# Performance work log

Measured on AMD Instinct MI355X. Metric: run time of the kernel, lower is better.

The kernel has to match this reference:

```python
import jax, jax.numpy as jnp
import numpy as np

MUL = 128
LS = (0, 1, 2, 3, 4)
LMAX = 4
DIM = MUL * sum(2 * l + 1 for l in LS)   # 3200
NUM_IRREPS = MUL * len(LS)               # 640
NUM_M = [MUL * (LMAX + 1 - m) for m in range(LMAX + 1)]
N = 16384


def _expm(A, order=24, squarings=10):
    A = A / (2.0 ** squarings)
    E = np.eye(A.shape[0])
    T = np.eye(A.shape[0])
    for k in range(1, order):
        T = T @ A / k
        E = E + T
    for _ in range(squarings):
        E = E @ E
    return E


def _su2_generators(j):
    m = np.arange(-j, j)
    raising = np.diag(-np.sqrt(j * (j + 1) - m * (m + 1)), k=-1).astype(complex)
    m = np.arange(-j + 1, j + 1)
    lowering = np.diag(np.sqrt(j * (j + 1) - m * (m - 1)), k=1).astype(complex)
    m = np.arange(-j, j + 1)
    return np.stack([0.5 * (raising + lowering), np.diag(1j * m), -0.5j * (raising - lowering)])


def _q_real_to_complex(l):
    q = np.zeros((2 * l + 1, 2 * l + 1), dtype=complex)
    for m in range(-l, 0):
        q[l + m, l + abs(m)] = 1 / np.sqrt(2)
        q[l + m, l - abs(m)] = -1j / np.sqrt(2)
    q[l, l] = 1.0
    for m in range(1, l + 1):
        q[l + m, l + abs(m)] = (-1) ** m / np.sqrt(2)
        q[l + m, l - abs(m)] = 1j * (-1) ** m / np.sqrt(2)
    return (-1j) ** l * q


def _so3_generators(l):
    X = _su2_generators(l)
    Q = _q_real_to_complex(l)
    return np.real(np.conj(Q.T)[None] @ X @ Q[None])


def _J(l):
    # J_l = pi rotation about (x+y)/sqrt(2): conjugates z_rot (y-axis) into the beta (x-axis) rotation,
    # reproducing e3nn's _Jd used in wigner_D = Z(a) J Z(b) J Z(g).
    X = _so3_generators(l)
    return _expm(np.pi * (X[0] + X[1]) / np.sqrt(2.0))


JMAT = {l: jnp.asarray(_J(l), dtype=jnp.float32) for l in LS if l > 0}


def _build_mask():
    mask = np.zeros((LMAX + 1, DIM), dtype=bool)
    cur = 0
    for l in LS:
        for k in range(MUL):
            base = cur + k * (2 * l + 1)
            for m in range(l + 1):
                if m == 0:
                    mask[0, base + l] = True
                else:
                    mask[m, base + l + m] = True
                    mask[m, base + l - m] = True
        cur += MUL * (2 * l + 1)
    return mask


_MASK = _build_mask()
IDX = [np.nonzero(_MASK[m])[0] for m in range(LMAX + 1)]  # same layout for in and out irreps


def _z_rot(angle, l):
    d = 2 * l + 1
    freqs = jnp.arange(l, -l - 1, -1, dtype=angle.dtype)
    c = jnp.cos(freqs * angle[:, None])
    s = jnp.sin(freqs * angle[:, None])
    i = jnp.arange(d)
    M = jnp.zeros((angle.shape[0], d, d), angle.dtype)
    M = M.at[:, i, i].set(c)
    M = M.at[:, i, d - 1 - i].add(s)
    return M


def _wigner(l, alpha, beta, gamma):
    J = JMAT[l].astype(alpha.dtype)
    return _z_rot(alpha, l) @ J @ _z_rot(beta, l) @ J @ _z_rot(gamma, l)


def _forward(x, R, fc0_w, fc0_b, w_ms):
    n = x.shape[0]
    # xyz_to_angles(R[:, [1, 2, 0]])
    v = jnp.stack([R[:, 1], R[:, 2], R[:, 0]], axis=-1)
    v = v / jnp.clip(jnp.linalg.norm(v, axis=-1, keepdims=True), 1e-12)
    v = jnp.clip(v, -1.0, 1.0)
    beta = jnp.arccos(v[:, 1])
    alpha = jnp.arctan2(v[:, 0], v[:, 2])
    gamma = jnp.zeros_like(alpha)
    rots = {l: _wigner(l, alpha, beta, gamma) for l in LS if l > 0}
    # rotate input blocks; the l=0 block of x_rot stays zero (exactly as the torch source)
    parts = []
    off = 0
    for l in LS:
        d = 2 * l + 1
        size = MUL * d
        if l == 0:
            parts.append(jnp.zeros((n, size), x.dtype))
        else:
            blk = x[:, off:off + size].reshape(n, MUL, d)
            parts.append(jnp.einsum('nji,nmj->nmi', rots[l], blk).reshape(n, size))
        off += size
    x_rot = jnp.concatenate(parts, axis=1)
    out = jnp.zeros((n, DIM), x.dtype)
    # m = 0 path (radial_emb=False => w = ones, a no-op multiply)
    out = out.at[:, IDX[0]].add(x_rot[:, IDX[0]] @ fc0_w.T + fc0_b)
    # m >= 1 SO(2) paths
    for m in range(1, LMAX + 1):
        co = NUM_M[m]
        seg = x_rot[:, IDX[m]].reshape(n, 2, co)
        y = jnp.einsum('nct,ot->nco', seg, w_ms[m - 1])  # (n, 2, 2*co)
        re = y[:, 0, :co] - y[:, 1, co:]
        im = y[:, 0, co:] + y[:, 1, :co]
        out = out.at[:, IDX[m]].add(jnp.stack((re, im), axis=1).reshape(n, -1))
    # rotate output blocks (l=0 untouched)
    parts = []
    off = 0
    for l in LS:
        d = 2 * l + 1
        size = MUL * d
        blk = out[:, off:off + size]
        if l > 0:
            blk = jnp.einsum('nji,nmj->nmi', rots[l], blk.reshape(n, MUL, d)).reshape(n, size)
        parts.append(blk)
        off += size
    return jnp.concatenate(parts, axis=1)


def setup_inputs() -> dict:
    key = jax.random.key(0)
    ks = jax.random.split(key, 8)
    x = jax.random.normal(ks[0], (N, DIM), jnp.float32)
    R = jax.random.normal(ks[1], (N, 3), jnp.float32)
    fc0_w = jax.random.normal(ks[2], (NUM_IRREPS, NUM_IRREPS), jnp.float32) / np.float32(np.sqrt(NUM_IRREPS))
    fc0_b = jnp.zeros((NUM_IRREPS,), jnp.float32)
    w1 = jax.random.normal(ks[3], (2 * NUM_M[1], NUM_M[1]), jnp.float32) / np.float32(np.sqrt(2.0 * NUM_M[1]))
    w2 = jax.random.normal(ks[4], (2 * NUM_M[2], NUM_M[2]), jnp.float32) / np.float32(np.sqrt(2.0 * NUM_M[2]))
    w3 = jax.random.normal(ks[5], (2 * NUM_M[3], NUM_M[3]), jnp.float32) / np.float32(np.sqrt(2.0 * NUM_M[3]))
    w4 = jax.random.normal(ks[6], (2 * NUM_M[4], NUM_M[4]), jnp.float32) / np.float32(np.sqrt(2.0 * NUM_M[4]))
    return {"x": x, "R": R, "fc0_w": fc0_w, "fc0_b": fc0_b, "w1": w1, "w2": w2, "w3": w3, "w4": w4}


def reference(x, R, fc0_w, fc0_b, w1, w2, w3, w4):
    return _forward(x, R, fc0_w, fc0_b, (w1, w2, w3, w4))
```

## Files before the change

### kernel.cpp

```cpp
#include <hip/hip_runtime.h>
#include <hip/hip_bf16.h>
#include <math.h>

#define N_ROWS 16384
#define DIM    3200

using short8  = __attribute__((ext_vector_type(8))) short;
using floatx4 = __attribute__((ext_vector_type(4))) float;

__device__ const int c_K [5] = {640, 1024, 768, 512, 256};
__device__ const int c_UO[5] = {0, 640, 1664, 2432, 2944};
__device__ const int c_WO[5] = {0, 409600, 1458176, 2048000, 2310144};
__device__ const int c_mOf[25]  = {0,0,0,0,0, 1,1,1,1,1,1,1,1, 2,2,2,2,2,2, 3,3,3,3, 4,4};
__device__ const int c_ntOf[25] = {0,1,2,3,4, 0,1,2,3,4,5,6,7, 0,1,2,3,4,5, 0,1,2,3, 0,1};

__device__ __forceinline__ constexpr int joff_of(int l) { return l==1 ? 0 : l==2 ? 9 : l==3 ? 34 : 83; }
__device__ __forceinline__ constexpr int gO(int m)      { return m==1 ? 640 : m==2 ? 1664 : m==3 ? 2432 : 2944; }

__global__ __launch_bounds__(128) void build_J(float* __restrict__ Jout)
{
    const int l = blockIdx.x + 1;
    const int d = 2*l + 1;
    const int dd = d*d;
    const int tid = threadIdx.x;
    __shared__ double Qr[81], Qi[81], Xr[81], Xi[81];
    __shared__ double M1r[81], M1i[81];
    __shared__ double Am[81], Em[81], Tm[81], Tn[81];

    if (tid == 0) {
        for (int e = 0; e < dd; ++e) { Qr[e]=0; Qi[e]=0; Xr[e]=0; Xi[e]=0; }
        const double jj = (double)l;
        for (int i = 0; i < d-1; ++i) {
            double mm = -jj + (double)i;
            Xr[(i+1)*d + i] += 0.5 * (-sqrt(jj*(jj+1.0) - mm*(mm+1.0)));
            double m2 = -jj + 1.0 + (double)i;
            Xr[i*d + (i+1)] += 0.5 * ( sqrt(jj*(jj+1.0) - m2*(m2-1.0)));
        }
        for (int i = 0; i < d; ++i) Xi[i*d + i] = -jj + (double)i;
        const double is2 = 1.0 / sqrt(2.0);
        for (int mm = -l; mm < 0; ++mm) {
            int r = l + mm;
            Qr[r*d + (l - mm)] = is2;
            Qi[r*d + (l + mm)] = -is2;
        }
        Qr[l*d + l] = 1.0;
        for (int mm = 1; mm <= l; ++mm) {
            int r = l + mm;
            double sgn = (mm & 1) ? -1.0 : 1.0;
            Qr[r*d + (l + mm)] = sgn * is2;
            Qi[r*d + (l - mm)] = sgn * is2;
        }
        double fr, fi;
        switch (l & 3) {
            case 0: fr = 1;  fi = 0;  break;
            case 1: fr = 0;  fi = -1; break;
            case 2: fr = -1; fi = 0;  break;
            default: fr = 0; fi = 1;  break;
        }
        for (int e = 0; e < dd; ++e) {
            double qr = Qr[e], qi = Qi[e];
            Qr[e] = qr*fr - qi*fi;
            Qi[e] = qr*fi + qi*fr;
        }
    }
    __syncthreads();
    const int i = (d > 0) ? tid / d : 0;
    const int j = (d > 0) ? tid % d : 0;
    if (tid < dd) {
        double ar = 0, ai = 0;
        for (int k = 0; k < d; ++k) {
            double xr = Xr[i*d+k], xi = Xi[i*d+k];
            double qr = Qr[k*d+j], qi = Qi[k*d+j];
            ar += xr*qr - xi*qi;
            ai += xr*qi + xi*qr;
        }
        M1r[tid] = ar; M1i[tid] = ai;
    }
    __syncthreads();
    if (tid < dd) {
        double ar = 0;
        for (int k = 0; k < d; ++k)
            ar += Qr[k*d+i]*M1r[k*d+j] + Qi[k*d+i]*M1i[k*d+j];
        const double scale = 3.14159265358979323846 / sqrt(2.0) / 1024.0;
        Am[tid] = ar * scale;
        Em[tid] = (i == j) ? 1.0 : 0.0;
        Tm[tid] = (i == j) ? 1.0 : 0.0;
    }
    __syncthreads();
    for (int k = 1; k < 24; ++k) {
        if (tid < dd) {
            double s = 0;
            for (int b = 0; b < d; ++b) s += Tm[i*d+b] * Am[b*d+j];
            Tn[tid] = s / (double)k;
        }
        __syncthreads();
        if (tid < dd) { Tm[tid] = Tn[tid]; Em[tid] += Tn[tid]; }
        __syncthreads();
    }
    for (int s = 0; s < 10; ++s) {
        if (tid < dd) {
            double v = 0;
            for (int b = 0; b < d; ++b) v += Em[i*d+b] * Em[b*d+j];
            Tn[tid] = v;
        }
        __syncthreads();
        if (tid < dd) Em[tid] = Tn[tid];
        __syncthreads();
    }
    if (tid < dd) Jout[joff_of(l) + tid] = (float)Em[tid];
}

__global__ __launch_bounds__(256) void prep_w(
    const float* __restrict__ fc0_w,
    const float* __restrict__ w1, const float* __restrict__ w2,
    const float* __restrict__ w3, const float* __restrict__ w4,
    __hip_bfloat16* __restrict__ Wall)
{
    const int m = blockIdx.y;
    const int idx = blockIdx.x * 256 + threadIdx.x;
    if (m == 0) {
        if (idx < 640*640) Wall[idx] = __float2bfloat16(fc0_w[idx]);
        return;
    }
    const int co = 128 * (5 - m);
    const int C  = 2 * co;
    if (idx >= C*C) return;
    const float* wm = (m==1) ? w1 : (m==2) ? w2 : (m==3) ? w3 : w4;
    const int jj = idx / C;
    const int tt = idx - jj * C;
    float v;
    if (jj < co) {
        v = (tt < co) ? wm[jj*co + tt] : -wm[(co + jj)*co + (tt - co)];
    } else {
        v = (tt < co) ? wm[jj*co + tt] :  wm[(jj - co)*co + (tt - co)];
    }
    Wall[c_WO[m] + idx] = __float2bfloat16(v);
}

template<int L>
__device__ __forceinline__ void rot_channel(const float* xs, const float* Dm,
                                            __hip_bfloat16* Urow, int k)
{
    constexpr int d = 2*L + 1;
    const float* Dl = Dm + joff_of(L);
    const int xoff = 128*L*L + k*d;
    float y[d];
#pragma unroll
    for (int q = 0; q < d; ++q) {
        float acc = 0.f;
#pragma unroll
        for (int j = 0; j < d; ++j) acc += Dl[j*d + q] * xs[xoff + j];
        y[q] = acc;
    }
#pragma unroll
    for (int q = 0; q < d; ++q) {
        const int mp = q - L;
        int g;
        if (mp == 0) g = L*128 + k;
        else {
            const int mm = mp < 0 ? -mp : mp;
            g = gO(mm) + 2*((L - mm)*128 + k) + (mp > 0 ? 1 : 0);
        }
        Urow[g] = __float2bfloat16(y[q]);
    }
}

template<int L>
__device__ __forceinline__ void unrot_channel(const __hip_bfloat16* ys, const float* Dm,
                                              float* orow, int k)
{
    constexpr int d = 2*L + 1;
    float yv[d];
#pragma unroll
    for (int q = 0; q < d; ++q) {
        const int mp = q - L;
        int g;
        if (mp == 0) g = L*128 + k;
        else {
            const int mm = mp < 0 ? -mp : mp;
            g = gO(mm) + 2*((L - mm)*128 + k) + (mp > 0 ? 1 : 0);
        }
        yv[q] = __bfloat162float(ys[g]);
    }
    const float* Dl = Dm + joff_of(L);
    const int ob = 128*L*L + k*d;
#pragma unroll
    for (int i = 0; i < d; ++i) {
        float acc = 0.f;
#pragma unroll
        for (int j = 0; j < d; ++j) acc += Dl[j*d + i] * yv[j];
        orow[ob + i] = acc;
    }
}

__global__ __launch_bounds__(256) void rot_gather(
    const float* __restrict__ x, const float* __restrict__ R,
    const float* __restrict__ Jws, float* __restrict__ Dws,
    __hip_bfloat16* __restrict__ U)
{
    const int row = blockIdx.x;
    const int tid = threadIdx.x;
    __shared__ __align__(16) float xs[DIM];
    __shared__ __align__(16) __hip_bfloat16 Urow[DIM];
    __shared__ float Jl[164], Ptmp[164], Dm[164];
    __shared__ float cA[5], sA[5], cB[5], sB[5];

    float r0 = R[row*3+0], r1 = R[row*3+1], r2 = R[row*3+2];
    float nrm = sqrtf(r0*r0 + r1*r1 + r2*r2);
    nrm = fmaxf(nrm, 1e-12f);
    float vx = r1/nrm, vy = r2/nrm, vz = r0/nrm;
    vx = fminf(1.f, fmaxf(-1.f, vx));
    vy = fminf(1.f, fmaxf(-1.f, vy));
    vz = fminf(1.f, fmaxf(-1.f, vz));
    float beta  = acosf(vy);
    float alpha = atan2f(vx, vz);

    if (tid < 164) Jl[tid] = Jws[tid];
    if (tid < 5) {
        float s, c;
        sincosf(alpha * (float)tid, &s, &c); sA[tid] = s; cA[tid] = c;
        sincosf(beta  * (float)tid, &s, &c); sB[tid] = s; cB[tid] = c;
    }
    {
        const float4* xg = (const float4*)(x + (size_t)row*DIM);
        float4* xl = (float4*)xs;
        for (int i = tid; i < DIM/4; i += 256) xl[i] = xg[i];
    }
    __syncthreads();

    int l = 0, base = 0;
    if (tid < 164) {
        if (tid < 9)       { l = 1; base = 0;  }
        else if (tid < 34) { l = 2; base = 9;  }
        else if (tid < 83) { l = 3; base = 34; }
        else               { l = 4; base = 83; }
        const int d = 2*l + 1;
        const int loc = tid - base;
        const int i = loc / d, j = loc - (loc/d)*d;
        const float* Jp = Jl + base;
        float acc = 0.f;
        for (int b = 0; b < d; ++b) {
            int f = l - b;
            float cb = cB[f < 0 ? -f : f];
            float sb = (b >= l) ? sB[b-l] : -sB[l-b];
            acc += (Jp[i*d+b]*cb + Jp[i*d + (d-1-b)]*sb) * Jp[b*d+j];
        }
        Ptmp[tid] = acc;
    }
    __syncthreads();
    if (tid < 164) {
        const int d = 2*l + 1;
        const int loc = tid - base;
        const int i = loc / d, j = loc - (loc/d)*d;
        int f = l - i;
        float ca = cA[f < 0 ? -f : f];
        float sa = (f > 0) ? sA[f] : ((f < 0) ? -sA[-f] : 0.f);
        float v = ca * Ptmp[tid] + sa * Ptmp[base + (d-1-i)*d + j];
        Dm[tid] = v;
        Dws[(size_t)row*164 + tid] = v;
    }
    __syncthreads();

    for (int c = tid; c < 640; c += 256) {
        int ll = c >> 7, k = c & 127;
        switch (ll) {
            case 0: Urow[k] = __float2bfloat16(0.f); break;
            case 1: rot_channel<1>(xs, Dm, Urow, k); break;
            case 2: rot_channel<2>(xs, Dm, Urow, k); break;
            case 3: rot_channel<3>(xs, Dm, Urow, k); break;
            case 4: rot_channel<4>(xs, Dm, Urow, k); break;
        }
    }
    __syncthreads();
    {
        uint4* ug = (uint4*)(U + (size_t)row*DIM);
        const uint4* ul = (const uint4*)Urow;
        for (int i = tid; i < (DIM*2)/16; i += 256) ug[i] = ul[i];
    }
}

__device__ __forceinline__ void g2lds16(const void* g, void* l) {
    __builtin_amdgcn_global_load_lds(
        (const __attribute__((address_space(1))) void*)g,
        (__attribute__((address_space(3))) void*)l, 16, 0, 0);
}

__global__ __launch_bounds__(256) void gemm_bt(
    const __hip_bfloat16* __restrict__ U, const __hip_bfloat16* __restrict__ W,
    const float* __restrict__ bias, __hip_bfloat16* __restrict__ Y)
{
    const int by = blockIdx.y;
    const int m  = c_mOf[by];
    const int nt = c_ntOf[by];
    const int K  = c_K[m];
    const int row0 = blockIdx.x * 128;
    const __hip_bfloat16* Ablk = U + (size_t)row0*DIM + c_UO[m];
    const __hip_bfloat16* Bblk = W + c_WO[m] + (size_t)nt*128*K;
    __shared__ __align__(16) __hip_bfloat16 As[128*32];
    __shared__ __align__(16) __hip_bfloat16 Bs[128*32];
    const int tid  = threadIdx.x;
    const int lane = tid & 63, w = tid >> 6;
    const int frow = lane & 15, quad = lane >> 4;
    const int wm = (w >> 1)*64, wn = (w & 1)*64;

    floatx4 acc[4][4];
#pragma unroll
    for (int i = 0; i < 4; ++i)
#pragma unroll
        for (int j = 0; j < 4; ++j) acc[i][j] = (floatx4){0.f, 0.f, 0.f, 0.f};

    const int c1 = w*64 + lane;
    const int c2 = c1 + 256;
    for (int k0 = 0; k0 < K; k0 += 32) {
        g2lds16(Ablk + (size_t)(c1 >> 2)*DIM + k0 + (c1 & 3)*8, (char*)As + w*1024);
        g2lds16(Ablk + (size_t)(c2 >> 2)*DIM + k0 + (c2 & 3)*8, (char*)As + 4096 + w*1024);
        g2lds16(Bblk + (size_t)(c1 >> 2)*K   + k0 + (c1 & 3)*8, (char*)Bs + w*1024);
        g2lds16(Bblk + (size_t)(c2 >> 2)*K   + k0 + (c2 & 3)*8, (char*)Bs + 4096 + w*1024);
        __syncthreads();
        short8 a[4], b[4];
#pragma unroll
        for (int t = 0; t < 4; ++t) {
            a[t] = *(const short8*)((const char*)As + (((wm + t*16 + frow)*32 + quad*8) * 2));
            b[t] = *(const short8*)((const char*)Bs + (((wn + t*16 + frow)*32 + quad*8) * 2));
        }
#pragma unroll
        for (int i = 0; i < 4; ++i)
#pragma unroll
            for (int j = 0; j < 4; ++j)
                acc[i][j] = __builtin_amdgcn_mfma_f32_16x16x32_bf16(a[i], b[j], acc[i][j], 0, 0, 0);
        __syncthreads();
    }
#pragma unroll
    for (int i = 0; i < 4; ++i) {
        const int r0 = row0 + wm + i*16 + quad*4;
#pragma unroll
        for (int j = 0; j < 4; ++j) {
            const int n = wn + j*16 + frow;
            const float bv = (m == 0) ? bias[nt*128 + n] : 0.f;
            const size_t colg = (size_t)c_UO[m] + nt*128 + n;
#pragma unroll
            for (int r = 0; r < 4; ++r)
                Y[(size_t)(r0 + r)*DIM + colg] = __float2bfloat16(acc[i][j][r] + bv);
        }
    }
}

__global__ __launch_bounds__(256) void ungather_rot(
    const __hip_bfloat16* __restrict__ Y, const float* __restrict__ Dws,
    float* __restrict__ out)
{
    const int row = blockIdx.x;
    const int tid = threadIdx.x;
    __shared__ __align__(16) __hip_bfloat16 ys[DIM];
    __shared__ __align__(16) float orow[DIM];
    __shared__ float Dm[164];
    {
        const uint4* yg = (const uint4*)(Y + (size_t)row*DIM);
        uint4* yl = (uint4*)ys;
        for (int i = tid; i < (DIM*2)/16; i += 256) yl[i] = yg[i];
    }
    if (tid < 164) Dm[tid] = Dws[(size_t)row*164 + tid];
    __syncthreads();
    for (int c = tid; c < 640; c += 256) {
        int ll = c >> 7, k = c & 127;
        switch (ll) {
            case 0: orow[k] = __bfloat162float(ys[k]); break;
            case 1: unrot_channel<1>(ys, Dm, orow, k); break;
            case 2: unrot_channel<2>(ys, Dm, orow, k); break;
            case 3: unrot_channel<3>(ys, Dm, orow, k); break;
            case 4: unrot_channel<4>(ys, Dm, orow, k); break;
        }
    }
    __syncthreads();
    {
        float4* og = (float4*)(out + (size_t)row*DIM);
        const float4* ol = (const float4*)orow;
        for (int i = tid; i < DIM/4; i += 256) og[i] = ol[i];
    }
}

extern "C" void kernel_launch(void* const* d_in, const int* in_sizes, int n_in,
                              void* d_out, int out_size, void* d_ws, size_t ws_size,
                              hipStream_t stream)
{
    (void)in_sizes; (void)n_in; (void)out_size; (void)ws_size;
    const float* x     = (const float*)d_in[0];
    const float* R     = (const float*)d_in[1];
    const float* fc0_w = (const float*)d_in[2];
    const float* fc0_b = (const float*)d_in[3];
    const float* w1    = (const float*)d_in[4];
    const float* w2    = (const float*)d_in[5];
    const float* w3    = (const float*)d_in[6];
    const float* w4    = (const float*)d_in[7];
    float* out = (float*)d_out;

    char* ws = (char*)d_ws;
    float*          Jws  = (float*)ws;
    __hip_bfloat16* Wall = (__hip_bfloat16*)(ws + 1024);
    float*          Dws  = (float*)(ws + 4752384);
    __hip_bfloat16* U    = (__hip_bfloat16*)(ws + 15500288);
    __hip_bfloat16* Y    = (__hip_bfloat16*)(ws + 120357888);

    build_J    <<<dim3(4),        dim3(128), 0, stream>>>(Jws);
    prep_w     <<<dim3(4096, 5),  dim3(256), 0, stream>>>(fc0_w, w1, w2, w3, w4, Wall);
    rot_gather <<<dim3(N_ROWS),   dim3(256), 0, stream>>>(x, R, Jws, Dws, U);
    gemm_bt    <<<dim3(128, 25),  dim3(256), 0, stream>>>(U, Wall, fc0_b, Y);
    ungather_rot<<<dim3(N_ROWS),  dim3(256), 0, stream>>>(Y, Dws, out);
}
```

Before: 761.8 us.

## Split Wigner-D build into separate kernels and flatten rotation kernels to per-channel threads

Moves the per-row trig and Wigner-D construction out of rot_gather into two standalone kernels, build_trig and build_D. The rotate and unrotate kernels become one thread per (row, channel) that reads and writes global memory directly, with no LDS staging and no block barriers. The paired m/-m bf16 values are packed into single 32-bit stores and loads. This removes the serial D-matrix phase and the syncs inside each row block, but the direct per-thread global accesses are strided by channel width and may coalesce poorly.

```diff
diff --git a/kernel.cpp b/kernel.cpp
--- a/kernel.cpp
+++ b/kernel.cpp
@@ -64,8 +64,8 @@
         }
     }
     __syncthreads();
-    const int i = (d > 0) ? tid / d : 0;
-    const int j = (d > 0) ? tid % d : 0;
+    const int i = tid / d;
+    const int j = tid % d;
     if (tid < dd) {
         double ar = 0, ai = 0;
         for (int k = 0; k < d; ++k) {
@@ -137,74 +137,11 @@
     Wall[c_WO[m] + idx] = __float2bfloat16(v);
 }
 
-template<int L>
-__device__ __forceinline__ void rot_channel(const float* xs, const float* Dm,
-                                            __hip_bfloat16* Urow, int k)
-{
-    constexpr int d = 2*L + 1;
-    const float* Dl = Dm + joff_of(L);
-    const int xoff = 128*L*L + k*d;
-    float y[d];
-#pragma unroll
-    for (int q = 0; q < d; ++q) {
-        float acc = 0.f;
-#pragma unroll
-        for (int j = 0; j < d; ++j) acc += Dl[j*d + q] * xs[xoff + j];
-        y[q] = acc;
-    }
-#pragma unroll
-    for (int q = 0; q < d; ++q) {
-        const int mp = q - L;
-        int g;
-        if (mp == 0) g = L*128 + k;
-        else {
-            const int mm = mp < 0 ? -mp : mp;
-            g = gO(mm) + 2*((L - mm)*128 + k) + (mp > 0 ? 1 : 0);
-        }
-        Urow[g] = __float2bfloat16(y[q]);
-    }
-}
-
-template<int L>
-__device__ __forceinline__ void unrot_channel(const __hip_bfloat16* ys, const float* Dm,
-                                              float* orow, int k)
-{
-    constexpr int d = 2*L + 1;
-    float yv[d];
-#pragma unroll
-    for (int q = 0; q < d; ++q) {
-        const int mp = q - L;
-        int g;
-        if (mp == 0) g = L*128 + k;
-        else {
-            const int mm = mp < 0 ? -mp : mp;
-            g = gO(mm) + 2*((L - mm)*128 + k) + (mp > 0 ? 1 : 0);
-        }
-        yv[q] = __bfloat162float(ys[g]);
-    }
-    const float* Dl = Dm + joff_of(L);
-    const int ob = 128*L*L + k*d;
-#pragma unroll
-    for (int i = 0; i < d; ++i) {
-        float acc = 0.f;
-#pragma unroll
-        for (int j = 0; j < d; ++j) acc += Dl[j*d + i] * yv[j];
-        orow[ob + i] = acc;
-    }
-}
-
-__global__ __launch_bounds__(256) void rot_gather(
-    const float* __restrict__ x, const float* __restrict__ R,
-    const float* __restrict__ Jws, float* __restrict__ Dws,
-    __hip_bfloat16* __restrict__ U)
-{
-    const int row = blockIdx.x;
-    const int tid = threadIdx.x;
-    __shared__ __align__(16) float xs[DIM];
-    __shared__ __align__(16) __hip_bfloat16 Urow[DIM];
-    __shared__ float Jl[164], Ptmp[164], Dm[164];
-    __shared__ float cA[5], sA[5], cB[5], sB[5];
-
+__global__ __launch_bounds__(256) void build_trig(
+    const float* __restrict__ R, float* __restrict__ trig)
+{
+    const int row = blockIdx.x * 256 + threadIdx.x;
+    if (row >= N_ROWS) return;
     float r0 = R[row*3+0], r1 = R[row*3+1], r2 = R[row*3+2];
     float nrm = sqrtf(r0*r0 + r1*r1 + r2*r2);
     nrm = fmaxf(nrm, 1e-12f);
@@ -214,68 +151,122 @@
     vz = fminf(1.f, fmaxf(-1.f, vz));
     float beta  = acosf(vy);
     float alpha = atan2f(vx, vz);
-
-    if (tid < 164) Jl[tid] = Jws[tid];
-    if (tid < 5) {
+    float* t = trig + row*20;
+#pragma unroll
+    for (int m = 0; m < 5; ++m) {
         float s, c;
-        sincosf(alpha * (float)tid, &s, &c); sA[tid] = s; cA[tid] = c;
-        sincosf(beta  * (float)tid, &s, &c); sB[tid] = s; cB[tid] = c;
-    }
-    {
-        const float4* xg = (const float4*)(x + (size_t)row*DIM);
-        float4* xl = (float4*)xs;
-        for (int i = tid; i < DIM/4; i += 256) xl[i] = xg[i];
-    }
-    __syncthreads();
-
-    int l = 0, base = 0;
-    if (tid < 164) {
-        if (tid < 9)       { l = 1; base = 0;  }
-        else if (tid < 34) { l = 2; base = 9;  }
-        else if (tid < 83) { l = 3; base = 34; }
-        else               { l = 4; base = 83; }
-        const int d = 2*l + 1;
-        const int loc = tid - base;
-        const int i = loc / d, j = loc - (loc/d)*d;
-        const float* Jp = Jl + base;
+        sincosf(alpha * (float)m, &s, &c);
+        t[m] = c; t[5+m] = s;
+        sincosf(beta * (float)m, &s, &c);
+        t[10+m] = c; t[15+m] = s;
+    }
+}
+
+__global__ __launch_bounds__(256) void build_D(
+    const float* __restrict__ Jws, const float* __restrict__ trig,
+    float* __restrict__ Dws)
+{
+    const int gid = blockIdx.x * 256 + threadIdx.x;
+    if (gid >= N_ROWS * 164) return;
+    const int row = gid / 164;
+    const int e   = gid - row * 164;
+    int l, base;
+    if (e < 9)       { l = 1; base = 0;  }
+    else if (e < 34) { l = 2; base = 9;  }
+    else if (e < 83) { l = 3; base = 34; }
+    else             { l = 4; base = 83; }
+    const int d = 2*l + 1;
+    const int loc = e - base;
+    const int i = loc / d, j = loc - i*d;
+    const float* Jp = Jws + base;
+    const float* t  = trig + row*20;
+    float pij = 0.f, pdj = 0.f;
+    for (int b = 0; b < d; ++b) {
+        int f = l - b; int af = f < 0 ? -f : f;
+        float cb = t[10 + af];
+        float sb = (b >= l) ? t[15 + b - l] : -t[15 + l - b];
+        float zr  = Jp[i*d + b]*cb + Jp[i*d + (d-1-b)]*sb;
+        float zr2 = Jp[(d-1-i)*d + b]*cb + Jp[(d-1-i)*d + (d-1-b)]*sb;
+        float jb  = Jp[b*d + j];
+        pij += zr  * jb;
+        pdj += zr2 * jb;
+    }
+    int f = l - i; int af = f < 0 ? -f : f;
+    float ca = t[af];
+    float sa = (f > 0) ? t[5 + f] : ((f < 0) ? -t[5 + af] : 0.f);
+    Dws[gid] = ca * pij + sa * pdj;
+}
+
+template<int L>
+__device__ __forceinline__ void rot_one(const float* __restrict__ xr,
+                                        const float* __restrict__ Dl,
+                                        __hip_bfloat16* __restrict__ Urow, int k)
+{
+    constexpr int d = 2*L + 1;
+    float xv[d], y[d];
+    const float* xp = xr + 128*L*L + k*d;
+#pragma unroll
+    for (int j = 0; j < d; ++j) xv[j] = xp[j];
+#pragma unroll
+    for (int q = 0; q < d; ++q) {
         float acc = 0.f;
-        for (int b = 0; b < d; ++b) {
-            int f = l - b;
-            float cb = cB[f < 0 ? -f : f];
-            float sb = (b >= l) ? sB[b-l] : -sB[l-b];
-            acc += (Jp[i*d+b]*cb + Jp[i*d + (d-1-b)]*sb) * Jp[b*d+j];
-        }
-        Ptmp[tid] = acc;
-    }
-    __syncthreads();
-    if (tid < 164) {
-        const int d = 2*l + 1;
-        const int loc = tid - base;
-        const int i = loc / d, j = loc - (loc/d)*d;
-        int f = l - i;
-        float ca = cA[f < 0 ? -f : f];
-        float sa = (f > 0) ? sA[f] : ((f < 0) ? -sA[-f] : 0.f);
-        float v = ca * Ptmp[tid] + sa * Ptmp[base + (d-1-i)*d + j];
-        Dm[tid] = v;
-        Dws[(size_t)row*164 + tid] = v;
-    }
-    __syncthreads();
-
-    for (int c = tid; c < 640; c += 256) {
-        int ll = c >> 7, k = c & 127;
-        switch (ll) {
-            case 0: Urow[k] = __float2bfloat16(0.f); break;
-            case 1: rot_channel<1>(xs, Dm, Urow, k); break;
-            case 2: rot_channel<2>(xs, Dm, Urow, k); break;
-            case 3: rot_channel<3>(xs, Dm, Urow, k); break;
-            case 4: rot_channel<4>(xs, Dm, Urow, k); break;
-        }
-    }
-    __syncthreads();
-    {
-        uint4* ug = (uint4*)(U + (size_t)row*DIM);
-        const uint4* ul = (const uint4*)Urow;
-        for (int i = tid; i < (DIM*2)/16; i += 256) ug[i] = ul[i];
+#pragma unroll
+        for (int j = 0; j < d; ++j) acc += Dl[j*d + q] * xv[j];
+        y[q] = acc;
+    }
+    Urow[L*128 + k] = __float2bfloat16(y[L]);
+#pragma unroll
+    for (int m = 1; m <= L; ++m) {
+        unsigned short lo = __builtin_bit_cast(unsigned short, __float2bfloat16(y[L-m]));
+        unsigned short hi = __builtin_bit_cast(unsigned short, __float2bfloat16(y[L+m]));
+        unsigned int pack = ((unsigned int)hi << 16) | lo;
+        *(unsigned int*)(Urow + gO(m) + 2*((L-m)*128 + k)) = pack;
+    }
+}
+
+template<int L>
+__device__ __forceinline__ void unrot_one(const __hip_bfloat16* __restrict__ Yrow,
+                                          const float* __restrict__ Dl,
+                                          float* __restrict__ orow, int k)
+{
+    constexpr int d = 2*L + 1;
+    float yv[d];
+    yv[L] = __bfloat162float(Yrow[L*128 + k]);
+#pragma unroll
+    for (int m = 1; m <= L; ++m) {
+        unsigned int pack = *(const unsigned int*)(Yrow + gO(m) + 2*((L-m)*128 + k));
+        unsigned short lo = (unsigned short)(pack & 0xffffu);
+        unsigned short hi = (unsigned short)(pack >> 16);
+        yv[L-m] = __bfloat162float(__builtin_bit_cast(__hip_bfloat16, lo));
+        yv[L+m] = __bfloat162float(__builtin_bit_cast(__hip_bfloat16, hi));
+    }
+    float* op = orow + 128*L*L + k*d;
+#pragma unroll
+    for (int i = 0; i < d; ++i) {
+        float acc = 0.f;
+#pragma unroll
+        for (int j = 0; j < d; ++j) acc += Dl[j*d + i] * yv[j];
+        op[i] = acc;
+    }
+}
+
+__global__ __launch_bounds__(256) void rot_gather(
+    const float* __restrict__ x, const float* __restrict__ Dws,
+    __hip_bfloat16* __restrict__ U)
+{
+    const int gid = blockIdx.x * 256 + threadIdx.x;
+    const int row = gid / 640;
+    const int c   = gid - row * 640;
+    const int l = c >> 7, k = c & 127;
+    const float* xr = x + (size_t)row * DIM;
+    __hip_bfloat16* Urow = U + (size_t)row * DIM;
+    const float* Dm = Dws + (size_t)row * 164;
+    switch (l) {
+        case 0: Urow[k] = __float2bfloat16(0.f); break;
+        case 1: rot_one<1>(xr, Dm + 0,  Urow, k); break;
+        case 2: rot_one<2>(xr, Dm + 9,  Urow, k); break;
+        case 3: rot_one<3>(xr, Dm + 34, Urow, k); break;
+        case 4: rot_one<4>(xr, Dm + 83, Urow, k); break;
     }
 }
 
@@ -349,33 +340,19 @@
     const __hip_bfloat16* __restrict__ Y, const float* __restrict__ Dws,
     float* __restrict__ out)
 {
-    const int row = blockIdx.x;
-    const int tid = threadIdx.x;
-    __shared__ __align__(16) __hip_bfloat16 ys[DIM];
-    __shared__ __align__(16) float orow[DIM];
-    __shared__ float Dm[164];
-    {
-        const uint4* yg = (const uint4*)(Y + (size_t)row*DIM);
-        uint4* yl = (uint4*)ys;
-        for (int i = tid; i < (DIM*2)/16; i += 256) yl[i] = yg[i];
-    }
-    if (tid < 164) Dm[tid] = Dws[(size_t)row*164 + tid];
-    __syncthreads();
-    for (int c = tid; c < 640; c += 256) {
-        int ll = c >> 7, k = c & 127;
-        switch (ll) {
-            case 0: orow[k] = __bfloat162float(ys[k]); break;
-            case 1: unrot_channel<1>(ys, Dm, orow, k); break;
-            case 2: unrot_channel<2>(ys, Dm, orow, k); break;
-            case 3: unrot_channel<3>(ys, Dm, orow, k); break;
-            case 4: unrot_channel<4>(ys, Dm, orow, k); break;
-        }
-    }
-    __syncthreads();
-    {
-        float4* og = (float4*)(out + (size_t)row*DIM);
-        const float4* ol = (const float4*)orow;
-        for (int i = tid; i < DIM/4; i += 256) og[i] = ol[i];
+    const int gid = blockIdx.x * 256 + threadIdx.x;
+    const int row = gid / 640;
+    const int c   = gid - row * 640;
+    const int l = c >> 7, k = c & 127;
+    const __hip_bfloat16* Yrow = Y + (size_t)row * DIM;
+    float* orow = out + (size_t)row * DIM;
+    const float* Dm = Dws + (size_t)row * 164;
+    switch (l) {
+        case 0: orow[k] = __bfloat162float(Yrow[k]); break;
+        case 1: unrot_one<1>(Yrow, Dm + 0,  orow, k); break;
+        case 2: unrot_one<2>(Yrow, Dm + 9,  orow, k); break;
+        case 3: unrot_one<3>(Yrow, Dm + 34, orow, k); break;
+        case 4: unrot_one<4>(Yrow, Dm + 83, orow, k); break;
     }
 }
 
@@ -400,10 +377,13 @@
     float*          Dws  = (float*)(ws + 4752384);
     __hip_bfloat16* U    = (__hip_bfloat16*)(ws + 15500288);
     __hip_bfloat16* Y    = (__hip_bfloat16*)(ws + 120357888);
-
-    build_J    <<<dim3(4),        dim3(128), 0, stream>>>(Jws);
-    prep_w     <<<dim3(4096, 5),  dim3(256), 0, stream>>>(fc0_w, w1, w2, w3, w4, Wall);
-    rot_gather <<<dim3(N_ROWS),   dim3(256), 0, stream>>>(x, R, Jws, Dws, U);
-    gemm_bt    <<<dim3(128, 25),  dim3(256), 0, stream>>>(U, Wall, fc0_b, Y);
-    ungather_rot<<<dim3(N_ROWS),  dim3(256), 0, stream>>>(Y, Dws, out);
-}
+    float*          trig = (float*)(ws + 120357888);
+
+    build_J     <<<dim3(4),         dim3(128), 0, stream>>>(Jws);
+    prep_w      <<<dim3(4096, 5),   dim3(256), 0, stream>>>(fc0_w, w1, w2, w3, w4, Wall);
+    build_trig  <<<dim3(64),        dim3(256), 0, stream>>>(R, trig);
+    build_D     <<<dim3(10496),     dim3(256), 0, stream>>>(Jws, trig, Dws);
+    rot_gather  <<<dim3(40960),     dim3(256), 0, stream>>>(x, Dws, U);
+    gemm_bt     <<<dim3(128, 25),   dim3(256), 0, stream>>>(U, Wall, fc0_b, Y);
+    ungather_rot<<<dim3(40960),     dim3(256), 0, stream>>>(Y, Dws, out);
+}
```

Result: faster. 678.9 us (-10.9%).
